# Performance work log

Hardware: AMD Instinct MI355X
Metric: run time of the kernel (lower is better)

## Reference

```python
import jax, jax.numpy as jnp
import numpy as np

N = 10000      # nodes
E = 160000     # edges (before self-loops)
H = 2          # ATTN_HEADS
D_IN = 256
C1 = 256       # hidden_channels per head in conv1
C2 = 512       # per-head channels in conv2 (hardcoded 512 in module)
OUT = 3


def setup_inputs():
    key = jax.random.key(0)
    ks = jax.random.split(key, 20)
    rn = lambda k, s, sc=0.05: jax.random.normal(k, s, jnp.float32) * sc
    return {
        "x": jax.random.normal(ks[0], (N, D_IN), jnp.float32),
        "edge_index": jax.random.randint(ks[1], (2, E), 0, N),
        # conv1: lin_src/lin_dst [D_IN, H*C1], attention vecs [H, C1], bias [H*C1]
        "w1s": rn(ks[2], (D_IN, H * C1)), "w1d": rn(ks[3], (D_IN, H * C1)),
        "a1s": rn(ks[4], (H, C1)), "a1d": rn(ks[5], (H, C1)), "b1": rn(ks[6], (H * C1,)),
        # conv2: input dim H*C1 -> [H*C1, H*C2]
        "w2s": rn(ks[7], (H * C1, H * C2)), "w2d": rn(ks[8], (H * C1, H * C2)),
        "a2s": rn(ks[9], (H, C2)), "a2d": rn(ks[10], (H, C2)), "b2": rn(ks[11], (H * C2,)),
        # MLP head
        "wf1": rn(ks[12], (H * C2, 128)), "bf1": rn(ks[13], (128,)),
        "gamma": jnp.ones((128,), jnp.float32), "beta": jnp.zeros((128,), jnp.float32),
        "wf2": rn(ks[14], (128, OUT)), "bf2": rn(ks[15], (OUT,)),
    }


def gat_layer(x, src, dst, Ws, Wd, att_s, att_d, b, n):
    h, c = att_s.shape
    xs = (x @ Ws).reshape(n, h, c)                      # [N,H,C] source messages
    xd = (x @ Wd).reshape(n, h, c)
    a_s = (xs * att_s).sum(-1)                          # [N,H]
    a_d = (xd * att_d).sum(-1)
    e = a_s[src] + a_d[dst]                             # [E,H]
    e = jnp.where(e > 0, e, 0.2 * e)                    # leaky_relu(0.2)
    m = jax.lax.stop_gradient(jax.ops.segment_max(e, dst, num_segments=n))
    alpha = jnp.exp(e - m[dst])
    denom = jax.ops.segment_sum(alpha, dst, num_segments=n)
    alpha = alpha / denom[dst]                          # segment softmax over dst
    out = jax.ops.segment_sum(xs[src] * alpha[..., None], dst, num_segments=n)
    return out.reshape(n, h * c) + b                    # concat heads + bias


def reference(x, edge_index, w1s, w1d, a1s, a1d, b1, w2s, w2d, a2s, a2d, b2,
              wf1, bf1, gamma, beta, wf2, bf2):
    loops = jnp.arange(N, dtype=edge_index.dtype)
    src = jnp.concatenate([edge_index[0], loops])       # add self-loops (PyG default)
    dst = jnp.concatenate([edge_index[1], loops])
    h = jax.nn.relu(gat_layer(x, src, dst, w1s, w1d, a1s, a1d, b1, N))
    h = jax.nn.relu(gat_layer(h, src, dst, w2s, w2d, a2s, a2d, b2, N))
    h = h @ wf1 + bf1
    mean = h.mean(0)
    var = ((h - mean) ** 2).mean(0)
    h = gamma * (h - mean) * jax.lax.rsqrt(var + 1e-5) + beta
    h = jax.nn.relu(h)
    h = h @ wf2 + bf2
    return jax.nn.log_softmax(h, axis=-1)
```

## Files before the change

### kernel.cpp

```cpp
#include <hip/hip_runtime.h>
#include <cstdint>
#include <cstddef>


typedef unsigned short u16;
typedef __bf16 bf16x8 __attribute__((ext_vector_type(8)));
typedef float f32x4 __attribute__((ext_vector_type(4)));
typedef unsigned short u16x8 __attribute__((ext_vector_type(8)));

__device__ __forceinline__ u16 f2b(float f) {
  union { float f; uint32_t u; } c; c.f = f;
  uint32_t u = c.u;
  return (u16)((u + 0x7FFFu + ((u >> 16) & 1u)) >> 16);
}
__device__ __forceinline__ float b2f(u16 h) {
  union { uint32_t u; float f; } c; c.u = ((uint32_t)h) << 16;
  return c.f;
}

__device__ __forceinline__ void async16(const void* g, void* l) {
  __builtin_amdgcn_global_load_lds((const __attribute__((address_space(1))) void*)g,
                                   (__attribute__((address_space(3))) void*)l, 16, 0, 0);
}

__device__ __forceinline__ float2 edge_w(const float4& as, const float4& ad) {
  float e0 = as.x + ad.z; e0 = e0 > 0.f ? e0 : 0.2f * e0;
  float e1 = as.y + ad.w; e1 = e1 > 0.f ? e1 : 0.2f * e1;
  return make_float2(__expf(e0), __expf(e1));
}

__device__ __forceinline__ void transpose_tile(const float* __restrict__ W, u16* __restrict__ WT,
                                               int K, int NC, int b, int t,
                                               u16 (*tile)[66]) {
  int tn = NC >> 6;
  int ti = b / tn, tj = b - ti * tn;
  int col = t & 63, r0 = t >> 6;
  const float* src = W + (size_t)(ti * 64) * NC + tj * 64;
#pragma unroll
  for (int i = 0; i < 16; i++) {
    int r = r0 + i * 4;
    tile[r][col] = f2b(src[(size_t)r * NC + col]);
  }
  __syncthreads();
  u16* dst = WT + (size_t)(tj * 64) * K + ti * 64;
#pragma unroll
  for (int i = 0; i < 16; i++) {
    int r = r0 + i * 4;
    dst[(size_t)r * K + col] = tile[col][r];
  }
}

__global__ __launch_bounds__(256) void prep(
    const float* __restrict__ x,
    const float* __restrict__ w1s, const float* __restrict__ w1d,
    const float* __restrict__ w2s, const float* __restrict__ w2d,
    const float* __restrict__ wf1,
    const float* __restrict__ a1s, const float* __restrict__ a1d,
    const float* __restrict__ a2s, const float* __restrict__ a2d,
    u16* __restrict__ xb, u16* __restrict__ w1T, u16* __restrict__ w2T,
    u16* __restrict__ wf1T, float* __restrict__ V1, float* __restrict__ V2,
    uint32_t* __restrict__ arena, int arena_nwords, int za,
    uint32_t* __restrict__ g1pad, int g1w, int zg1,
    uint32_t* __restrict__ g2pad, int g2w,
    int N) {
  __shared__ u16 tile[64][66];
  int b = blockIdx.x, t = threadIdx.x;
  const int R0 = 32;
  const int R1 = R0 + 128;
  const int R2 = R1 + 32;
  const int R3 = R2 + 256;
  const int R4 = R3 + 512;
  const int R5 = R4 + N / 4;
  const int R6 = R5 + za;
  const int R7 = R6 + zg1;

  if (b < R0) {
    transpose_tile(w1s, w1T, 256, 512, b, t, tile);
  } else if (b < R1) {
    transpose_tile(w2s, w2T, 512, 1024, b - R0, t, tile);
  } else if (b < R2) {
    transpose_tile(wf1, wf1T, 1024, 128, b - R1, t, tile);
  } else if (b < R3) {
    int wv = t >> 6, lane = t & 63;
    int u = (b - R2) * 4 + wv;
    int k = u >> 2, which = (u >> 1) & 1, h = u & 1;
    const float* W = which ? w1d : w1s;
    const float* att = which ? a1d : a1s;
    float s = 0.f;
#pragma unroll
    for (int c = lane; c < 256; c += 64) s += W[k * 512 + h * 256 + c] * att[h * 256 + c];
#pragma unroll
    for (int o = 32; o > 0; o >>= 1) s += __shfl_down(s, o);
    if (lane == 0) V1[k * 4 + which * 2 + h] = s;
  } else if (b < R4) {
    int wv = t >> 6, lane = t & 63;
    int u = (b - R3) * 4 + wv;
    int k = u >> 2, which = (u >> 1) & 1, h = u & 1;
    const float* W = which ? w2d : w2s;
    const float* att = which ? a2d : a2s;
    float s = 0.f;
#pragma unroll
    for (int c = lane; c < 512; c += 64) s += W[k * 1024 + h * 512 + c] * att[h * 512 + c];
#pragma unroll
    for (int o = 32; o > 0; o >>= 1) s += __shfl_down(s, o);
    if (lane == 0) V2[k * 4 + which * 2 + h] = s;
  } else if (b < R5) {
    int r = (b - R4) * 4 + (t >> 6);
    int c = (t & 63) * 4;
    float4 xv = *(const float4*)(x + (size_t)r * 256 + c);
    ushort4 st;
    st.x = f2b(xv.x); st.y = f2b(xv.y); st.z = f2b(xv.z); st.w = f2b(xv.w);
    *(ushort4*)(xb + (size_t)r * 256 + c) = st;
  } else if (b < R6) {
    int idx = (b - R5) * 256 + t;
    if (idx < arena_nwords) arena[idx] = 0u;
  } else if (b < R7) {
    int idx = (b - R6) * 256 + t;
    if (idx < g1w) g1pad[idx] = 0u;
  } else {
    int idx = (b - R7) * 256 + t;
    if (idx < g2w) g2pad[idx] = 0u;
  }
}

__global__ __launch_bounds__(256) void fill_a(const int* __restrict__ srcs,
                                              const int* __restrict__ dsts,
                                              int* __restrict__ cursor, int* __restrict__ csr,
                                              const float* __restrict__ X,
                                              const float* __restrict__ V,
                                              float* __restrict__ A, int N, int E, int FB) {
  int b = blockIdx.x, t = threadIdx.x;
  if (b < FB) {
    int i = b * 256 + t;
    if (i < N) {
      csr[(size_t)i * 64] = i;
    } else if (i < N + E) {
      int e = i - N;
      int d = dsts[e];
      int slot = atomicAdd(&cursor[d], 1) + 1;
      if (slot < 64) csr[(size_t)d * 64 + slot] = srcs[e];
    }
    return;
  }
  int node = (b - FB) * 4 + (t >> 6);
  int lane = t & 63;
  if (node >= N) return;
  const float* xr = X + (size_t)node * 256;
  float s0 = 0, s1 = 0, s2 = 0, s3 = 0;
  {
    int k = lane * 4;
    float4 xv = *(const float4*)(xr + k);
    float xe[4] = {xv.x, xv.y, xv.z, xv.w};
#pragma unroll
    for (int j = 0; j < 4; j++) {
      float4 v = ((const float4*)V)[k + j];
      s0 += xe[j] * v.x; s1 += xe[j] * v.y; s2 += xe[j] * v.z; s3 += xe[j] * v.w;
    }
  }
#pragma unroll
  for (int o = 32; o > 0; o >>= 1) {
    s0 += __shfl_down(s0, o); s1 += __shfl_down(s1, o);
    s2 += __shfl_down(s2, o); s3 += __shfl_down(s3, o);
  }
  if (lane == 0) ((float4*)A)[node] = make_float4(s0, s1, s2, s3);
}

__global__ __launch_bounds__(256) void agg1(const u16* __restrict__ xs,
                                            const float* __restrict__ a,
                                            const int* __restrict__ cursor,
                                            const int* __restrict__ csr,
                                            u16* __restrict__ g, int N) {
  int v = blockIdx.x * 8 + (threadIdx.x >> 5);
  if (v >= N) return;
  int c0 = (threadIdx.x & 31) * 8;
  const int* seg = csr + (size_t)v * 64;
  int cnt = min(cursor[v], 63) + 1;
  const float4* a4 = (const float4*)a;
  float4 adv = a4[v];
  float h0[8], h1[8];
#pragma unroll
  for (int j = 0; j < 8; j++) { h0[j] = 0.f; h1[j] = 0.f; }
  float den0 = 0.f, den1 = 0.f;
  int i = 0;
  for (; i + 4 <= cnt; i += 4) {
    int4 s4 = *(const int4*)(seg + i);
    float4 aa0 = a4[s4.x], aa1 = a4[s4.y], aa2 = a4[s4.z], aa3 = a4[s4.w];
    u16x8 x0 = *(const u16x8*)(xs + (size_t)s4.x * 256 + c0);
    u16x8 x1 = *(const u16x8*)(xs + (size_t)s4.y * 256 + c0);
    u16x8 x2 = *(const u16x8*)(xs + (size_t)s4.z * 256 + c0);
    u16x8 x3 = *(const u16x8*)(xs + (size_t)s4.w * 256 + c0);
    float2 w0 = edge_w(aa0, adv), w1 = edge_w(aa1, adv);
    float2 w2 = edge_w(aa2, adv), w3 = edge_w(aa3, adv);
    den0 += w0.x + w1.x + w2.x + w3.x;
    den1 += w0.y + w1.y + w2.y + w3.y;
#pragma unroll
    for (int j = 0; j < 8; j++) {
      float f0 = b2f(x0[j]), f1 = b2f(x1[j]), f2 = b2f(x2[j]), f3 = b2f(x3[j]);
      h0[j] += w0.x * f0 + w1.x * f1 + w2.x * f2 + w3.x * f3;
      h1[j] += w0.y * f0 + w1.y * f1 + w2.y * f2 + w3.y * f3;
    }
  }
  for (; i < cnt; i++) {
    int s = seg[i];
    float2 w = edge_w(a4[s], adv);
    den0 += w.x; den1 += w.y;
    u16x8 xv = *(const u16x8*)(xs + (size_t)s * 256 + c0);
#pragma unroll
    for (int j = 0; j < 8; j++) {
      float f = b2f(xv[j]);
      h0[j] += w.x * f;
      h1[j] += w.y * f;
    }
  }
  float r0 = 1.f / den0, r1 = 1.f / den1;
  u16x8 o0v, o1v;
#pragma unroll
  for (int j = 0; j < 8; j++) {
    o0v[j] = f2b(h0[j] * r0);
    o1v[j] = f2b(h1[j] * r1);
  }
  u16* grow = g + (size_t)v * 512;
  *(u16x8*)(grow + c0) = o0v;
  *(u16x8*)(grow + 256 + c0) = o1v;
}

__global__ __launch_bounds__(256) void agg2(const u16* __restrict__ xs,
                                            const float* __restrict__ a,
                                            const int* __restrict__ cursor,
                                            const int* __restrict__ csr,
                                            u16* __restrict__ g, int N) {
  int v = blockIdx.x * 4 + (threadIdx.x >> 6);
  if (v >= N) return;
  int c0 = (threadIdx.x & 63) * 8;
  const int* seg = csr + (size_t)v * 64;
  int cnt = min(cursor[v], 63) + 1;
  const float4* a4 = (const float4*)a;
  float4 adv = a4[v];
  float h0[8], h1[8];
#pragma unroll
  for (int j = 0; j < 8; j++) { h0[j] = 0.f; h1[j] = 0.f; }
  float den0 = 0.f, den1 = 0.f;
  int i = 0;
  for (; i + 4 <= cnt; i += 4) {
    int4 s4 = *(const int4*)(seg + i);
    float4 aa0 = a4[s4.x], aa1 = a4[s4.y], aa2 = a4[s4.z], aa3 = a4[s4.w];
    u16x8 x0 = *(const u16x8*)(xs + (size_t)s4.x * 512 + c0);
    u16x8 x1 = *(const u16x8*)(xs + (size_t)s4.y * 512 + c0);
    u16x8 x2 = *(const u16x8*)(xs + (size_t)s4.z * 512 + c0);
    u16x8 x3 = *(const u16x8*)(xs + (size_t)s4.w * 512 + c0);
    float2 w0 = edge_w(aa0, adv), w1 = edge_w(aa1, adv);
    float2 w2 = edge_w(aa2, adv), w3 = edge_w(aa3, adv);
    den0 += w0.x + w1.x + w2.x + w3.x;
    den1 += w0.y + w1.y + w2.y + w3.y;
#pragma unroll
    for (int j = 0; j < 8; j++) {
      float f0 = b2f(x0[j]), f1 = b2f(x1[j]), f2 = b2f(x2[j]), f3 = b2f(x3[j]);
      h0[j] += w0.x * f0 + w1.x * f1 + w2.x * f2 + w3.x * f3;
      h1[j] += w0.y * f0 + w1.y * f1 + w2.y * f2 + w3.y * f3;
    }
  }
  for (; i < cnt; i++) {
    int s = seg[i];
    float2 w = edge_w(a4[s], adv);
    den0 += w.x; den1 += w.y;
    u16x8 xv = *(const u16x8*)(xs + (size_t)s * 512 + c0);
#pragma unroll
    for (int j = 0; j < 8; j++) {
      float f = b2f(xv[j]);
      h0[j] += w.x * f;
      h1[j] += w.y * f;
    }
  }
  float r0 = 1.f / den0, r1 = 1.f / den1;
  u16x8 o0v, o1v;
#pragma unroll
  for (int j = 0; j < 8; j++) {
    o0v[j] = f2b(h0[j] * r0);
    o1v[j] = f2b(h1[j] * r1);
  }
  u16* grow = g + (size_t)v * 1024;
  *(u16x8*)(grow + c0) = o0v;
  *(u16x8*)(grow + 512 + c0) = o1v;
}

template <int OMODE, bool A2OUT>
__global__ __launch_bounds__(256) void gemm_bf16(const u16* __restrict__ A, int lda, int aZ,
                                                 const u16* __restrict__ BT, int ldb, int bZ,
                                                 const float* __restrict__ bias, int biasZ,
                                                 int relu, void* __restrict__ Cv, int ldc,
                                                 size_t cZ, int K, float* __restrict__ a2out,
                                                 const float* __restrict__ Vfold,
                                                 float* __restrict__ sums, int Nrows) {
  __shared__ u16 Asl[2][128 * 32];
  __shared__ u16 Bsl[2][128 * 32];
  int tid = threadIdx.x;
  int wave = tid >> 6, lane = tid & 63;
  int wr = wave >> 1, wc = wave & 1;
  int lr = lane & 15, quad = lane >> 4;
  size_t row0 = (size_t)blockIdx.y * 128;
  size_t n0 = (size_t)blockIdx.x * 128;
  int zq = blockIdx.z;
  if (OMODE == 1) {
    A += (size_t)zq * aZ;
    BT += (size_t)zq * bZ;
    bias += (size_t)zq * biasZ;
  }

  f32x4 acc[4][4];
#pragma unroll
  for (int i = 0; i < 4; i++)
#pragma unroll
    for (int j = 0; j < 4; j++) acc[i][j] = (f32x4){0.f, 0.f, 0.f, 0.f};

  int ra = tid >> 2;
  int ca = (tid & 3) * 8;
  const u16* gA = A + (row0 + ra) * lda + ca;
  const u16* gB = BT + (n0 + ra) * ldb + ca;
  int lbase = (tid & 192) * 8;

  async16(gA, &Asl[0][lbase]);
  async16(gA + (size_t)64 * lda, &Asl[0][lbase + 2048]);
  async16(gB, &Bsl[0][lbase]);
  async16(gB + (size_t)64 * ldb, &Bsl[0][lbase + 2048]);
  __syncthreads();

  int nIter = K >> 5;
  for (int it = 0; it < nIter; it++) {
    int cur = it & 1;
    if (it + 1 < nIter) {
      int kn = (it + 1) * 32;
      async16(gA + kn, &Asl[1 - cur][lbase]);
      async16(gA + (size_t)64 * lda + kn, &Asl[1 - cur][lbase + 2048]);
      async16(gB + kn, &Bsl[1 - cur][lbase]);
      async16(gB + (size_t)64 * ldb + kn, &Bsl[1 - cur][lbase + 2048]);
    }
    bf16x8 av[4], bv[4];
#pragma unroll
    for (int i = 0; i < 4; i++)
      av[i] = *(const bf16x8*)&Asl[cur][(wr * 64 + i * 16 + lr) * 32 + quad * 8];
#pragma unroll
    for (int j = 0; j < 4; j++)
      bv[j] = *(const bf16x8*)&Bsl[cur][(wc * 64 + j * 16 + lr) * 32 + quad * 8];
#pragma unroll
    for (int i = 0; i < 4; i++)
#pragma unroll
      for (int j = 0; j < 4; j++)
        acc[i][j] = __builtin_amdgcn_mfma_f32_16x16x32_bf16(av[i], bv[j], acc[i][j], 0, 0, 0);
    __syncthreads();
  }

  size_t crow = row0 + wr * 64 + quad * 4;
  size_t ccol = n0 + wc * 64 + lr;
  if (OMODE == 1) {
    float bj[4];
#pragma unroll
    for (int j = 0; j < 4; j++) bj[j] = bias[ccol + j * 16];
    float4 vr[4];
    if (A2OUT) {
#pragma unroll
      for (int j = 0; j < 4; j++)
        vr[j] = ((const float4*)Vfold)[(size_t)zq * cZ + ccol + j * 16];
    }
    u16* C = (u16*)Cv + (size_t)zq * cZ;
#pragma unroll
    for (int i = 0; i < 4; i++) {
#pragma unroll
      for (int r = 0; r < 4; r++) {
        float pa0 = 0.f, pa1 = 0.f, pa2 = 0.f, pa3 = 0.f;
#pragma unroll
        for (int j = 0; j < 4; j++) {
          float val = acc[i][j][r] + bj[j];
          if (relu) val = fmaxf(val, 0.f);
          C[(crow + i * 16 + r) * ldc + ccol + j * 16] = f2b(val);
          if (A2OUT) {
            pa0 += val * vr[j].x; pa1 += val * vr[j].y;
            pa2 += val * vr[j].z; pa3 += val * vr[j].w;
          }
        }
        if (A2OUT) {
#pragma unroll
          for (int o = 8; o > 0; o >>= 1) {
            pa0 += __shfl_down(pa0, o); pa1 += __shfl_down(pa1, o);
            pa2 += __shfl_down(pa2, o); pa3 += __shfl_down(pa3, o);
          }
          if (lr == 0) {
            float* ap = a2out + (crow + i * 16 + r) * 4;
            atomicAdd(ap + 0, pa0); atomicAdd(ap + 1, pa1);
            atomicAdd(ap + 2, pa2); atomicAdd(ap + 3, pa3);
          }
        }
      }
    }
  } else {
    float* C = (float*)Cv;
    float s1[4] = {0.f, 0.f, 0.f, 0.f}, s2[4] = {0.f, 0.f, 0.f, 0.f};
#pragma unroll
    for (int i = 0; i < 4; i++)
#pragma unroll
      for (int r = 0; r < 4; r++) {
        size_t row = crow + i * 16 + r;
#pragma unroll
        for (int j = 0; j < 4; j++) {
          float v = acc[i][j][r];
          C[row * ldc + ccol + j * 16] = v;
          if ((int)row < Nrows) { s1[j] += v; s2[j] += v * v; }
        }
      }
#pragma unroll
    for (int j = 0; j < 4; j++) {
#pragma unroll
      for (int o = 16; o < 64; o <<= 1) {
        s1[j] += __shfl_down(s1[j], o);
        s2[j] += __shfl_down(s2[j], o);
      }
    }
    if (quad == 0) {
#pragma unroll
      for (int j = 0; j < 4; j++) {
        atomicAdd(&sums[ccol + j * 16], s1[j]);
        atomicAdd(&sums[128 + ccol + j * 16], s2[j]);
      }
    }
  }
}

__global__ __launch_bounds__(256) void head_kernel(const float* __restrict__ z,
                                                   const float* __restrict__ sums,
                                                   const float* __restrict__ gamma,
                                                   const float* __restrict__ beta,
                                                   const float* __restrict__ wf2,
                                                   const float* __restrict__ bf2,
                                                   float* __restrict__ out, int N) {
  int v = blockIdx.x * 4 + (threadIdx.x >> 6);
  if (v >= N) return;
  int lane = threadIdx.x & 63;
  float inv = 1.f / (float)N;
  float p0 = 0.f, p1 = 0.f, p2 = 0.f;
#pragma unroll
  for (int half = 0; half < 2; half++) {
    int j = lane + half * 64;
    float mean = sums[j] * inv;
    float var = sums[128 + j] * inv - mean * mean;
    float rstd = rsqrtf(var + 1e-5f);
    float h = z[(size_t)v * 128 + j];
    h = gamma[j] * (h - mean) * rstd + beta[j];
    h = h > 0.f ? h : 0.f;
    p0 += h * wf2[j * 3 + 0];
    p1 += h * wf2[j * 3 + 1];
    p2 += h * wf2[j * 3 + 2];
  }
#pragma unroll
  for (int o = 32; o > 0; o >>= 1) {
    p0 += __shfl_down(p0, o);
    p1 += __shfl_down(p1, o);
    p2 += __shfl_down(p2, o);
  }
  if (lane == 0) {
    float l0 = p0 + bf2[0], l1 = p1 + bf2[1], l2 = p2 + bf2[2];
    float mx = fmaxf(l0, fmaxf(l1, l2));
    float lse = mx + logf(__expf(l0 - mx) + __expf(l1 - mx) + __expf(l2 - mx));
    out[v * 3 + 0] = l0 - lse;
    out[v * 3 + 1] = l1 - lse;
    out[v * 3 + 2] = l2 - lse;
  }
}

extern "C" void kernel_launch(void* const* d_in, const int* in_sizes, int n_in,
                              void* d_out, int out_size, void* d_ws, size_t ws_size,
                              hipStream_t stream) {
  const float* x     = (const float*)d_in[0];
  const int*   ei    = (const int*)d_in[1];
  const float* w1s   = (const float*)d_in[2];
  const float* w1d   = (const float*)d_in[3];
  const float* a1s   = (const float*)d_in[4];
  const float* a1d   = (const float*)d_in[5];
  const float* b1    = (const float*)d_in[6];
  const float* w2s   = (const float*)d_in[7];
  const float* w2d   = (const float*)d_in[8];
  const float* a2s   = (const float*)d_in[9];
  const float* a2d   = (const float*)d_in[10];
  const float* b2    = (const float*)d_in[11];
  const float* wf1   = (const float*)d_in[12];
  const float* gamma = (const float*)d_in[14];
  const float* beta  = (const float*)d_in[15];
  const float* wf2   = (const float*)d_in[16];
  const float* bf2   = (const float*)d_in[17];
  float* out = (float*)d_out;

  const int N = in_sizes[0] / 256;
  const int E = in_sizes[1] / 2;
  const int Mpad = ((N + 127) / 128) * 128;
  (void)n_in; (void)out_size; (void)ws_size;

  char* ws = (char*)d_ws;
  size_t off = 0;
  auto alloc = [&](size_t bytes) -> char* {
    off = (off + 255) & ~(size_t)255;
    char* p = ws + off;
    off += bytes;
    return p;
  };
  u16* xb    = (u16*)alloc((size_t)N * 256 * 2);
  u16* w1T   = (u16*)alloc((size_t)512 * 256 * 2);
  u16* w2T   = (u16*)alloc((size_t)1024 * 512 * 2);
  u16* wf1T  = (u16*)alloc((size_t)128 * 1024 * 2);
  u16* g1    = (u16*)alloc((size_t)Mpad * 512 * 2);
  u16* h1    = (u16*)alloc((size_t)Mpad * 512 * 2);
  u16* g2    = (u16*)alloc((size_t)Mpad * 1024 * 2);
  u16* h2    = (u16*)alloc((size_t)Mpad * 1024 * 2);
  float* z   = (float*)alloc((size_t)Mpad * 128 * 4);
  float* a1  = (float*)alloc((size_t)N * 16);
  float* V1  = (float*)alloc(256 * 16);
  float* V2  = (float*)alloc(512 * 16);
  int* csr   = (int*)alloc((size_t)N * 64 * 4);
  size_t curB = (size_t)N * 4;
  size_t a2B = (size_t)Mpad * 16;
  size_t arenaB = curB + a2B + 1024;
  char* arena = alloc(arenaB);
  int* cursor = (int*)arena;
  float* a2   = (float*)(arena + curB);
  float* sums = (float*)(arena + curB + a2B);

  int arena_nwords = (int)(arenaB / 4);
  int za  = (arena_nwords + 255) / 256;
  int g1w = (Mpad - N) * 512 * 2 / 4;
  int zg1 = (g1w + 255) / 256;
  int g2w = (Mpad - N) * 1024 * 2 / 4;
  int zg2 = (g2w + 255) / 256;
  int prep_blocks = 32 + 128 + 32 + 256 + 512 + N / 4 + za + zg1 + zg2;

  prep<<<prep_blocks, 256, 0, stream>>>(
      x, w1s, w1d, w2s, w2d, wf1, a1s, a1d, a2s, a2d,
      xb, w1T, w2T, wf1T, V1, V2,
      (uint32_t*)arena, arena_nwords, za,
      (uint32_t*)(g1 + (size_t)N * 512), g1w, zg1,
      (uint32_t*)(g2 + (size_t)N * 1024), g2w, N);

  const int* srcs = ei;
  const int* dsts = ei + E;

  int FB = (N + E + 255) / 256;
  fill_a<<<FB + (N + 3) / 4, 256, 0, stream>>>(srcs, dsts, cursor, csr, x, V1, a1, N, E, FB);

  int mt = Mpad / 128;

  agg1<<<(N + 7) / 8, 256, 0, stream>>>(xb, a1, cursor, csr, g1, N);
  gemm_bf16<1, true><<<dim3(2, mt, 2), 256, 0, stream>>>(
      g1, 512, 256, w1T, 256, 256 * 256, b1, 256, 1, h1, 512, 256, 256, a2, V2,
      nullptr, 0);
  agg2<<<(N + 3) / 4, 256, 0, stream>>>(h1, a2, cursor, csr, g2, N);
  gemm_bf16<1, false><<<dim3(4, mt, 2), 256, 0, stream>>>(
      g2, 1024, 512, w2T, 512, 512 * 512, b2, 512, 1, h2, 1024, 512, 512, nullptr, nullptr,
      nullptr, 0);
  gemm_bf16<0, false><<<dim3(1, mt, 1), 256, 0, stream>>>(
      h2, 1024, 0, wf1T, 1024, 0, b2 , 0, 0, z, 128, 0, 1024, nullptr, nullptr,
      sums, N);
  head_kernel<<<(N + 3) / 4, 256, 0, stream>>>(z, sums, gamma, beta, wf2, bf2, out, N);
}
```

Before: 232.9 us.

## Fuse final GEMM with batchnorm head via grid barrier, prefetch CSR indices

Replaces the final MLP GEMM plus separate head kernel with one kernel. It computes column sums, waits at a grid-wide atomic-counter barrier, then applies batchnorm, ReLU, the 3-way projection and log-softmax from registers. This removes the z buffer round trip and one launch. It depends on all 160 blocks being co-resident, otherwise the spin barrier can deadlock. The aggregation kernels also prefetch the next int4 of neighbor indices one iteration ahead to hide index-load latency.

```diff
diff --git a/kernel.cpp b/kernel.cpp
--- a/kernel.cpp
+++ b/kernel.cpp
@@ -181,9 +181,8 @@
 #pragma unroll
   for (int j = 0; j < 8; j++) { h0[j] = 0.f; h1[j] = 0.f; }
   float den0 = 0.f, den1 = 0.f;
-  int i = 0;
-  for (; i + 4 <= cnt; i += 4) {
-    int4 s4 = *(const int4*)(seg + i);
+
+  auto body = [&](int4 s4) {
     float4 aa0 = a4[s4.x], aa1 = a4[s4.y], aa2 = a4[s4.z], aa3 = a4[s4.w];
     u16x8 x0 = *(const u16x8*)(xs + (size_t)s4.x * 256 + c0);
     u16x8 x1 = *(const u16x8*)(xs + (size_t)s4.y * 256 + c0);
@@ -199,6 +198,19 @@
       h0[j] += w0.x * f0 + w1.x * f1 + w2.x * f2 + w3.x * f3;
       h1[j] += w0.y * f0 + w1.y * f1 + w2.y * f2 + w3.y * f3;
     }
+  };
+
+  int nb4 = cnt & ~3;
+  int i = 0;
+  if (nb4 > 0) {
+    int4 s4 = *(const int4*)(seg);
+    for (i = 4; i < nb4; i += 4) {
+      int4 nxt = *(const int4*)(seg + i);
+      body(s4);
+      s4 = nxt;
+    }
+    body(s4);
+    i = nb4;
   }
   for (; i < cnt; i++) {
     int s = seg[i];
@@ -240,9 +252,8 @@
 #pragma unroll
   for (int j = 0; j < 8; j++) { h0[j] = 0.f; h1[j] = 0.f; }
   float den0 = 0.f, den1 = 0.f;
-  int i = 0;
-  for (; i + 4 <= cnt; i += 4) {
-    int4 s4 = *(const int4*)(seg + i);
+
+  auto body = [&](int4 s4) {
     float4 aa0 = a4[s4.x], aa1 = a4[s4.y], aa2 = a4[s4.z], aa3 = a4[s4.w];
     u16x8 x0 = *(const u16x8*)(xs + (size_t)s4.x * 512 + c0);
     u16x8 x1 = *(const u16x8*)(xs + (size_t)s4.y * 512 + c0);
@@ -258,6 +269,19 @@
       h0[j] += w0.x * f0 + w1.x * f1 + w2.x * f2 + w3.x * f3;
       h1[j] += w0.y * f0 + w1.y * f1 + w2.y * f2 + w3.y * f3;
     }
+  };
+
+  int nb4 = cnt & ~3;
+  int i = 0;
+  if (nb4 > 0) {
+    int4 s4 = *(const int4*)(seg);
+    for (i = 4; i < nb4; i += 4) {
+      int4 nxt = *(const int4*)(seg + i);
+      body(s4);
+      s4 = nxt;
+    }
+    body(s4);
+    i = nb4;
   }
   for (; i < cnt; i++) {
     int s = seg[i];
@@ -283,14 +307,13 @@
   *(u16x8*)(grow + 512 + c0) = o1v;
 }
 
-template <int OMODE, bool A2OUT>
+template <bool A2OUT>
 __global__ __launch_bounds__(256) void gemm_bf16(const u16* __restrict__ A, int lda, int aZ,
                                                  const u16* __restrict__ BT, int ldb, int bZ,
                                                  const float* __restrict__ bias, int biasZ,
-                                                 int relu, void* __restrict__ Cv, int ldc,
+                                                 void* __restrict__ Cv, int ldc,
                                                  size_t cZ, int K, float* __restrict__ a2out,
-                                                 const float* __restrict__ Vfold,
-                                                 float* __restrict__ sums, int Nrows) {
+                                                 const float* __restrict__ Vfold) {
   __shared__ u16 Asl[2][128 * 32];
   __shared__ u16 Bsl[2][128 * 32];
   int tid = threadIdx.x;
@@ -300,11 +323,9 @@
   size_t row0 = (size_t)blockIdx.y * 128;
   size_t n0 = (size_t)blockIdx.x * 128;
   int zq = blockIdx.z;
-  if (OMODE == 1) {
-    A += (size_t)zq * aZ;
-    BT += (size_t)zq * bZ;
-    bias += (size_t)zq * biasZ;
-  }
+  A += (size_t)zq * aZ;
+  BT += (size_t)zq * bZ;
+  bias += (size_t)zq * biasZ;
 
   f32x4 acc[4][4];
 #pragma unroll
@@ -351,117 +372,185 @@
 
   size_t crow = row0 + wr * 64 + quad * 4;
   size_t ccol = n0 + wc * 64 + lr;
-  if (OMODE == 1) {
-    float bj[4];
-#pragma unroll
-    for (int j = 0; j < 4; j++) bj[j] = bias[ccol + j * 16];
-    float4 vr[4];
-    if (A2OUT) {
-#pragma unroll
-      for (int j = 0; j < 4; j++)
-        vr[j] = ((const float4*)Vfold)[(size_t)zq * cZ + ccol + j * 16];
-    }
-    u16* C = (u16*)Cv + (size_t)zq * cZ;
-#pragma unroll
-    for (int i = 0; i < 4; i++) {
-#pragma unroll
-      for (int r = 0; r < 4; r++) {
-        float pa0 = 0.f, pa1 = 0.f, pa2 = 0.f, pa3 = 0.f;
-#pragma unroll
-        for (int j = 0; j < 4; j++) {
-          float val = acc[i][j][r] + bj[j];
-          if (relu) val = fmaxf(val, 0.f);
-          C[(crow + i * 16 + r) * ldc + ccol + j * 16] = f2b(val);
-          if (A2OUT) {
-            pa0 += val * vr[j].x; pa1 += val * vr[j].y;
-            pa2 += val * vr[j].z; pa3 += val * vr[j].w;
-          }
-        }
+  float bj[4];
+#pragma unroll
+  for (int j = 0; j < 4; j++) bj[j] = bias[ccol + j * 16];
+  float4 vr[4];
+  if (A2OUT) {
+#pragma unroll
+    for (int j = 0; j < 4; j++)
+      vr[j] = ((const float4*)Vfold)[(size_t)zq * cZ + ccol + j * 16];
+  }
+  u16* C = (u16*)Cv + (size_t)zq * cZ;
+#pragma unroll
+  for (int i = 0; i < 4; i++) {
+#pragma unroll
+    for (int r = 0; r < 4; r++) {
+      float pa0 = 0.f, pa1 = 0.f, pa2 = 0.f, pa3 = 0.f;
+#pragma unroll
+      for (int j = 0; j < 4; j++) {
+        float val = fmaxf(acc[i][j][r] + bj[j], 0.f);
+        C[(crow + i * 16 + r) * ldc + ccol + j * 16] = f2b(val);
         if (A2OUT) {
-#pragma unroll
-          for (int o = 8; o > 0; o >>= 1) {
-            pa0 += __shfl_down(pa0, o); pa1 += __shfl_down(pa1, o);
-            pa2 += __shfl_down(pa2, o); pa3 += __shfl_down(pa3, o);
-          }
-          if (lr == 0) {
-            float* ap = a2out + (crow + i * 16 + r) * 4;
-            atomicAdd(ap + 0, pa0); atomicAdd(ap + 1, pa1);
-            atomicAdd(ap + 2, pa2); atomicAdd(ap + 3, pa3);
-          }
+          pa0 += val * vr[j].x; pa1 += val * vr[j].y;
+          pa2 += val * vr[j].z; pa3 += val * vr[j].w;
         }
       }
-    }
-  } else {
-    float* C = (float*)Cv;
-    float s1[4] = {0.f, 0.f, 0.f, 0.f}, s2[4] = {0.f, 0.f, 0.f, 0.f};
-#pragma unroll
-    for (int i = 0; i < 4; i++)
-#pragma unroll
-      for (int r = 0; r < 4; r++) {
-        size_t row = crow + i * 16 + r;
+      if (A2OUT) {
+#pragma unroll
+        for (int o = 8; o > 0; o >>= 1) {
+          pa0 += __shfl_down(pa0, o); pa1 += __shfl_down(pa1, o);
+          pa2 += __shfl_down(pa2, o); pa3 += __shfl_down(pa3, o);
+        }
+        if (lr == 0) {
+          float* ap = a2out + (crow + i * 16 + r) * 4;
+          atomicAdd(ap + 0, pa0); atomicAdd(ap + 1, pa1);
+          atomicAdd(ap + 2, pa2); atomicAdd(ap + 3, pa3);
+        }
+      }
+    }
+  }
+}
+
+__global__ __launch_bounds__(256) void gemm3_head(
+    const u16* __restrict__ A, const u16* __restrict__ BT,
+    float* __restrict__ sums, unsigned int* __restrict__ ctr,
+    const float* __restrict__ gamma, const float* __restrict__ beta,
+    const float* __restrict__ wf2, const float* __restrict__ bf2,
+    float* __restrict__ out, int N, int nBlocks) {
+  __shared__ u16 Asl[2][64 * 32];
+  __shared__ u16 Bsl[2][128 * 32];
+  __shared__ float part[2][64][3];
+  int tid = threadIdx.x;
+  int wave = tid >> 6, lane = tid & 63;
+  int wr = wave >> 1, wc = wave & 1;
+  int lr = lane & 15, quad = lane >> 4;
+  size_t row0 = (size_t)blockIdx.x * 64;
+
+  f32x4 acc[2][4];
+#pragma unroll
+  for (int i = 0; i < 2; i++)
+#pragma unroll
+    for (int j = 0; j < 4; j++) acc[i][j] = (f32x4){0.f, 0.f, 0.f, 0.f};
+
+  const u16* gA = A + (row0 + (tid >> 2)) * 1024 + (tid & 3) * 8;
+  const u16* gB = BT + (size_t)(tid >> 2) * 1024 + (tid & 3) * 8;
+  int lb = (tid & 192) * 8;
+
+  async16(gA, &Asl[0][lb]);
+  async16(gB, &Bsl[0][lb]);
+  async16(gB + 64 * 1024, &Bsl[0][2048 + lb]);
+  __syncthreads();
+
+  for (int it = 0; it < 32; it++) {
+    int cur = it & 1;
+    if (it + 1 < 32) {
+      int kn = (it + 1) * 32;
+      async16(gA + kn, &Asl[1 - cur][lb]);
+      async16(gB + kn, &Bsl[1 - cur][lb]);
+      async16(gB + 64 * 1024 + kn, &Bsl[1 - cur][2048 + lb]);
+    }
+    bf16x8 av[2], bv[4];
+#pragma unroll
+    for (int i = 0; i < 2; i++)
+      av[i] = *(const bf16x8*)&Asl[cur][(wr * 32 + i * 16 + lr) * 32 + quad * 8];
+#pragma unroll
+    for (int j = 0; j < 4; j++)
+      bv[j] = *(const bf16x8*)&Bsl[cur][(wc * 64 + j * 16 + lr) * 32 + quad * 8];
+#pragma unroll
+    for (int i = 0; i < 2; i++)
+#pragma unroll
+      for (int j = 0; j < 4; j++)
+        acc[i][j] = __builtin_amdgcn_mfma_f32_16x16x32_bf16(av[i], bv[j], acc[i][j], 0, 0, 0);
+    __syncthreads();
+  }
+
+  int ccol = wc * 64 + lr;
+  float s1[4] = {0.f, 0.f, 0.f, 0.f}, s2[4] = {0.f, 0.f, 0.f, 0.f};
+#pragma unroll
+  for (int i = 0; i < 2; i++)
+#pragma unroll
+    for (int r = 0; r < 4; r++) {
+      int row = (int)row0 + wr * 32 + i * 16 + quad * 4 + r;
+      if (row < N) {
 #pragma unroll
         for (int j = 0; j < 4; j++) {
           float v = acc[i][j][r];
-          C[row * ldc + ccol + j * 16] = v;
-          if ((int)row < Nrows) { s1[j] += v; s2[j] += v * v; }
+          s1[j] += v; s2[j] += v * v;
         }
       }
+    }
+#pragma unroll
+  for (int j = 0; j < 4; j++) {
+#pragma unroll
+    for (int o = 16; o < 64; o <<= 1) {
+      s1[j] += __shfl_down(s1[j], o);
+      s2[j] += __shfl_down(s2[j], o);
+    }
+  }
+  if (quad == 0) {
 #pragma unroll
     for (int j = 0; j < 4; j++) {
-#pragma unroll
-      for (int o = 16; o < 64; o <<= 1) {
-        s1[j] += __shfl_down(s1[j], o);
-        s2[j] += __shfl_down(s2[j], o);
+      atomicAdd(&sums[ccol + j * 16], s1[j]);
+      atomicAdd(&sums[128 + ccol + j * 16], s2[j]);
+    }
+  }
+
+  __syncthreads();
+  if (tid == 0) {
+    __threadfence();
+    atomicAdd(ctr, 1u);
+    while (__hip_atomic_load(ctr, __ATOMIC_ACQUIRE, __HIP_MEMORY_SCOPE_AGENT) <
+           (unsigned)nBlocks) {
+    }
+  }
+  __syncthreads();
+
+  float inv = 1.f / (float)N;
+  float mean[4], rstd[4], gm[4], bt[4], w3[4][3];
+#pragma unroll
+  for (int j = 0; j < 4; j++) {
+    int col = ccol + j * 16;
+    float sv = __hip_atomic_load(&sums[col], __ATOMIC_RELAXED, __HIP_MEMORY_SCOPE_AGENT);
+    float qv = __hip_atomic_load(&sums[128 + col], __ATOMIC_RELAXED, __HIP_MEMORY_SCOPE_AGENT);
+    mean[j] = sv * inv;
+    float var = qv * inv - mean[j] * mean[j];
+    rstd[j] = rsqrtf(var + 1e-5f);
+    gm[j] = gamma[col]; bt[j] = beta[col];
+    w3[j][0] = wf2[col * 3 + 0]; w3[j][1] = wf2[col * 3 + 1]; w3[j][2] = wf2[col * 3 + 2];
+  }
+#pragma unroll
+  for (int i = 0; i < 2; i++)
+#pragma unroll
+    for (int r = 0; r < 4; r++) {
+      float p0 = 0.f, p1 = 0.f, p2 = 0.f;
+#pragma unroll
+      for (int j = 0; j < 4; j++) {
+        float h = gm[j] * (acc[i][j][r] - mean[j]) * rstd[j] + bt[j];
+        h = fmaxf(h, 0.f);
+        p0 += h * w3[j][0]; p1 += h * w3[j][1]; p2 += h * w3[j][2];
       }
-    }
-    if (quad == 0) {
-#pragma unroll
-      for (int j = 0; j < 4; j++) {
-        atomicAdd(&sums[ccol + j * 16], s1[j]);
-        atomicAdd(&sums[128 + ccol + j * 16], s2[j]);
+#pragma unroll
+      for (int o = 8; o > 0; o >>= 1) {
+        p0 += __shfl_down(p0, o); p1 += __shfl_down(p1, o); p2 += __shfl_down(p2, o);
       }
-    }
-  }
-}
-
-__global__ __launch_bounds__(256) void head_kernel(const float* __restrict__ z,
-                                                   const float* __restrict__ sums,
-                                                   const float* __restrict__ gamma,
-                                                   const float* __restrict__ beta,
-                                                   const float* __restrict__ wf2,
-                                                   const float* __restrict__ bf2,
-                                                   float* __restrict__ out, int N) {
-  int v = blockIdx.x * 4 + (threadIdx.x >> 6);
-  if (v >= N) return;
-  int lane = threadIdx.x & 63;
-  float inv = 1.f / (float)N;
-  float p0 = 0.f, p1 = 0.f, p2 = 0.f;
-#pragma unroll
-  for (int half = 0; half < 2; half++) {
-    int j = lane + half * 64;
-    float mean = sums[j] * inv;
-    float var = sums[128 + j] * inv - mean * mean;
-    float rstd = rsqrtf(var + 1e-5f);
-    float h = z[(size_t)v * 128 + j];
-    h = gamma[j] * (h - mean) * rstd + beta[j];
-    h = h > 0.f ? h : 0.f;
-    p0 += h * wf2[j * 3 + 0];
-    p1 += h * wf2[j * 3 + 1];
-    p2 += h * wf2[j * 3 + 2];
-  }
-#pragma unroll
-  for (int o = 32; o > 0; o >>= 1) {
-    p0 += __shfl_down(p0, o);
-    p1 += __shfl_down(p1, o);
-    p2 += __shfl_down(p2, o);
-  }
-  if (lane == 0) {
-    float l0 = p0 + bf2[0], l1 = p1 + bf2[1], l2 = p2 + bf2[2];
-    float mx = fmaxf(l0, fmaxf(l1, l2));
-    float lse = mx + logf(__expf(l0 - mx) + __expf(l1 - mx) + __expf(l2 - mx));
-    out[v * 3 + 0] = l0 - lse;
-    out[v * 3 + 1] = l1 - lse;
-    out[v * 3 + 2] = l2 - lse;
+      if (lr == 0) {
+        int lrow = wr * 32 + i * 16 + quad * 4 + r;
+        part[wc][lrow][0] = p0; part[wc][lrow][1] = p1; part[wc][lrow][2] = p2;
+      }
+    }
+  __syncthreads();
+  if (tid < 64) {
+    int row = tid;
+    if ((int)row0 + row < N) {
+      float l0 = part[0][row][0] + part[1][row][0] + bf2[0];
+      float l1 = part[0][row][1] + part[1][row][1] + bf2[1];
+      float l2 = part[0][row][2] + part[1][row][2] + bf2[2];
+      float mx = fmaxf(l0, fmaxf(l1, l2));
+      float lse = mx + logf(__expf(l0 - mx) + __expf(l1 - mx) + __expf(l2 - mx));
+      float* orow = out + ((size_t)row0 + row) * 3;
+      orow[0] = l0 - lse; orow[1] = l1 - lse; orow[2] = l2 - lse;
+    }
   }
 }
 
@@ -508,18 +597,18 @@
   u16* h1    = (u16*)alloc((size_t)Mpad * 512 * 2);
   u16* g2    = (u16*)alloc((size_t)Mpad * 1024 * 2);
   u16* h2    = (u16*)alloc((size_t)Mpad * 1024 * 2);
-  float* z   = (float*)alloc((size_t)Mpad * 128 * 4);
   float* a1  = (float*)alloc((size_t)N * 16);
   float* V1  = (float*)alloc(256 * 16);
   float* V2  = (float*)alloc(512 * 16);
   int* csr   = (int*)alloc((size_t)N * 64 * 4);
   size_t curB = (size_t)N * 4;
   size_t a2B = (size_t)Mpad * 16;
-  size_t arenaB = curB + a2B + 1024;
+  size_t arenaB = curB + a2B + 1024 + 256;
   char* arena = alloc(arenaB);
   int* cursor = (int*)arena;
   float* a2   = (float*)(arena + curB);
   float* sums = (float*)(arena + curB + a2B);
+  unsigned int* ctr = (unsigned int*)(sums + 256);
 
   int arena_nwords = (int)(arenaB / 4);
   int za  = (arena_nwords + 255) / 256;
@@ -545,15 +634,11 @@
   int mt = Mpad / 128;
 
   agg1<<<(N + 7) / 8, 256, 0, stream>>>(xb, a1, cursor, csr, g1, N);
-  gemm_bf16<1, true><<<dim3(2, mt, 2), 256, 0, stream>>>(
-      g1, 512, 256, w1T, 256, 256 * 256, b1, 256, 1, h1, 512, 256, 256, a2, V2,
-      nullptr, 0);
+  gemm_bf16<true><<<dim3(2, mt, 2), 256, 0, stream>>>(
+      g1, 512, 256, w1T, 256, 256 * 256, b1, 256, h1, 512, 256, 256, a2, V2);
   agg2<<<(N + 3) / 4, 256, 0, stream>>>(h1, a2, cursor, csr, g2, N);
-  gemm_bf16<1, false><<<dim3(4, mt, 2), 256, 0, stream>>>(
-      g2, 1024, 512, w2T, 512, 512 * 512, b2, 512, 1, h2, 1024, 512, 512, nullptr, nullptr,
-      nullptr, 0);
-  gemm_bf16<0, false><<<dim3(1, mt, 1), 256, 0, stream>>>(
-      h2, 1024, 0, wf1T, 1024, 0, b2 , 0, 0, z, 128, 0, 1024, nullptr, nullptr,
-      sums, N);
-  head_kernel<<<(N + 3) / 4, 256, 0, stream>>>(z, sums, gamma, beta, wf2, bf2, out, N);
-}
+  gemm_bf16<false><<<dim3(4, mt, 2), 256, 0, stream>>>(
+      g2, 1024, 512, w2T, 512, 512 * 512, b2, 512, h2, 1024, 512, 512, nullptr, nullptr);
+  int nB3 = Mpad / 64;
+  gemm3_head<<<nB3, 256, 0, stream>>>(h2, wf1T, sums, ctr, gamma, beta, wf2, bf2, out, N, nB3);
+}
```

Measured after the change: 233.1 us. No clear change (+0.1%).
